# Optimization experiments

Measured on AMD Instinct MI355X. Metric: run time of the kernel, lower is better.

Reference implementation:

```python
import jax, jax.numpy as jnp
import numpy as np

N_NODES = 50000
N_EDGES = 800000
F_IN = 128          # num_features
F_HID = 128 * 3     # conv1 out
F_OUT = 256         # num_relations = num_criteria**2
N_CRIT = 16         # num_criteria


def setup_inputs() -> dict:
    key = jax.random.key(0)
    k_feat, k_edge, k_w1, k_w2 = jax.random.split(key, 4)
    features = jax.random.normal(k_feat, (N_NODES, F_IN), dtype=jnp.float32)
    edge_index = jax.random.randint(k_edge, (2, N_EDGES), 0, N_NODES, dtype=jnp.int32)
    # Glorot-ish init like dglnn.GraphConv
    W1 = jax.random.normal(k_w1, (F_IN, F_HID), dtype=jnp.float32) * (1.0 / np.sqrt(F_IN))
    b1 = jnp.zeros((F_HID,), dtype=jnp.float32)
    W2 = jax.random.normal(k_w2, (F_HID, F_OUT), dtype=jnp.float32) * (1.0 / np.sqrt(F_HID))
    b2 = jnp.zeros((F_OUT,), dtype=jnp.float32)
    return {"features": features, "W1": W1, "b1": b1, "W2": W2, "b2": b2,
            "edge_index": edge_index}


def reference(features, W1, b1, W2, b2, edge_index):
    src, dst = edge_index[0], edge_index[1]
    ones = jnp.ones((edge_index.shape[1],), dtype=features.dtype)
    # symmetric GCN norm with degrees clamped to min 1 (DGL norm='both')
    deg_out = jax.ops.segment_sum(ones, src, num_segments=N_NODES)
    deg_in = jax.ops.segment_sum(ones, dst, num_segments=N_NODES)
    out_norm = jnp.clip(deg_out, 1.0, None) ** -0.5   # [N]
    in_norm = jnp.clip(deg_in, 1.0, None) ** -0.5     # [N]

    def aggregate(h):
        # h: [N, d] -> D_in^{-1/2} A D_out^{-1/2} h  via edge gather + segment_sum
        msg = (h * out_norm[:, None])[src]                              # [E, d]
        return jax.ops.segment_sum(msg, dst, num_segments=N_NODES) * in_norm[:, None]

    # conv1: in(128) < out(384) -> aggregate first, then dense transform
    x = jax.nn.relu(aggregate(features) @ W1 + b1)      # [N, 384]
    # conv2: in(384) > out(256) -> dense transform first, then aggregate
    x = aggregate(x @ W2) + b2                          # [N, 256]
    return x.reshape(-1, N_CRIT, N_CRIT)                # [N, 16, 16]
```

## Files before the change

kernel.cpp:

```cpp
#include <hip/hip_runtime.h>
#include <hip/hip_bf16.h>

typedef float f32x4 __attribute__((ext_vector_type(4)));
typedef __bf16 bf16x8 __attribute__((ext_vector_type(8)));

#define NNODES 50000
#define NEDGES 800000
#define FIN 128
#define FHID 384
#define FOUT 256

#define SCAN_NB ((NNODES + 1023) / 1024)

__device__ __forceinline__ float bf_lo(unsigned u) { return __uint_as_float(u << 16); }
__device__ __forceinline__ float bf_hi(unsigned u) { return __uint_as_float(u & 0xffff0000u); }
__device__ __forceinline__ unsigned short f2bf(float f) {
  unsigned u = __float_as_uint(f);
  u += 0x7fffu + ((u >> 16) & 1u);
  return (unsigned short)(u >> 16);
}

__global__ void cvt_feat_kernel(const float* __restrict__ f,
                                const float* __restrict__ onorm,
                                unsigned short* __restrict__ o, int n4) {
  int i = blockIdx.x * blockDim.x + threadIdx.x;
  if (i >= n4) return;
  float4 v = *(const float4*)(f + (size_t)i * 4);
  float w = onorm[(i * 4) >> 7];
  ushort4 r;
  r.x = f2bf(v.x * w); r.y = f2bf(v.y * w);
  r.z = f2bf(v.z * w); r.w = f2bf(v.w * w);
  *(ushort4*)(o + (size_t)i * 4) = r;
}

__global__ void wt_kernel(const float* __restrict__ W, __bf16* __restrict__ Wt, int K, int Nw) {
  int i = blockIdx.x * blockDim.x + threadIdx.x;
  if (i >= K * Nw) return;
  int k = i / Nw, n = i % Nw;
  unsigned short b = f2bf(W[i]);
  Wt[(size_t)n * K + k] = *(__bf16*)&b;
}

__global__ void degree_kernel(const int* __restrict__ ei, int* __restrict__ dout, int* __restrict__ din) {
  int e = blockIdx.x * blockDim.x + threadIdx.x;
  if (e >= NEDGES) return;
  atomicAdd(&dout[ei[e]], 1);
  atomicAdd(&din[ei[NEDGES + e]], 1);
}

__global__ void norm_kernel(const int* __restrict__ dout, const int* __restrict__ din,
                            float* __restrict__ onorm, float* __restrict__ inorm) {
  int i = blockIdx.x * blockDim.x + threadIdx.x;
  if (i >= NNODES) return;
  int a = dout[i]; if (a < 1) a = 1;
  int b = din[i]; if (b < 1) b = 1;
  onorm[i] = rsqrtf((float)a);
  inorm[i] = rsqrtf((float)b);
}

__global__ __launch_bounds__(256) void scan_part1(const int* __restrict__ deg,
                                                  int* __restrict__ blocksums) {
  int b = blockIdx.x, t = threadIdx.x;
  int base = b * 1024 + t * 4;
  int s = 0;
  if (base + 4 <= NNODES) {
    int4 v = *(const int4*)(deg + base);
    s = v.x + v.y + v.z + v.w;
  } else {
    for (int j = 0; j < 4; ++j)
      if (base + j < NNODES) s += deg[base + j];
  }
  for (int d = 32; d >= 1; d >>= 1) s += __shfl_down(s, d, 64);
  __shared__ int ws[4];
  int lane = t & 63, w = t >> 6;
  if (lane == 0) ws[w] = s;
  __syncthreads();
  if (t == 0) blocksums[b] = ws[0] + ws[1] + ws[2] + ws[3];
}

__global__ void scan_mid(const int* __restrict__ bs, int* __restrict__ boff) {
  int t = threadIdx.x;
  int v = (t < SCAN_NB) ? bs[t] : 0;
  int x = v;
  for (int d = 1; d < 64; d <<= 1) {
    int y = __shfl_up(x, d, 64);
    if (t >= d) x += y;
  }
  if (t < SCAN_NB) boff[t] = x - v;
}

__global__ __launch_bounds__(256) void scan_part2(const int* __restrict__ deg,
                                                  const int* __restrict__ boff,
                                                  int* __restrict__ row_ptr,
                                                  int* __restrict__ cursor) {
  int b = blockIdx.x, t = threadIdx.x;
  int base = b * 1024 + t * 4;
  int v0 = 0, v1 = 0, v2 = 0, v3 = 0;
  if (base + 4 <= NNODES) {
    int4 v = *(const int4*)(deg + base);
    v0 = v.x; v1 = v.y; v2 = v.z; v3 = v.w;
  } else {
    if (base + 0 < NNODES) v0 = deg[base + 0];
    if (base + 1 < NNODES) v1 = deg[base + 1];
    if (base + 2 < NNODES) v2 = deg[base + 2];
    if (base + 3 < NNODES) v3 = deg[base + 3];
  }
  int s = v0 + v1 + v2 + v3;
  int x = s;
  int lane = t & 63, w = t >> 6;
  for (int d = 1; d < 64; d <<= 1) {
    int y = __shfl_up(x, d, 64);
    if (lane >= d) x += y;
  }
  __shared__ int ws[4];
  if (lane == 63) ws[w] = x;
  __syncthreads();
  int woff = 0;
  for (int i = 0; i < w; ++i) woff += ws[i];
  int off = boff[b] + woff + (x - s);
  if (base + 0 < NNODES) { row_ptr[base + 0] = off; cursor[base + 0] = off; off += v0; }
  if (base + 1 < NNODES) { row_ptr[base + 1] = off; cursor[base + 1] = off; off += v1; }
  if (base + 2 < NNODES) { row_ptr[base + 2] = off; cursor[base + 2] = off; off += v2; }
  if (base + 3 < NNODES) { row_ptr[base + 3] = off; cursor[base + 3] = off; off += v3; }
  if (base < NNODES && base + 4 >= NNODES) row_ptr[NNODES] = off;
}

__global__ void fill_kernel(const int* __restrict__ ei, int* __restrict__ cursor, int* __restrict__ csr) {
  int e = blockIdx.x * blockDim.x + threadIdx.x;
  if (e >= NEDGES) return;
  int d = ei[NEDGES + e];
  int pos = atomicAdd(&cursor[d], 1);
  csr[pos] = ei[e];
}

__global__ __launch_bounds__(256) void agg1_kernel(
    const int* __restrict__ row_ptr, const int* __restrict__ csr,
    const float* __restrict__ inorm, const unsigned short* __restrict__ featb,
    unsigned short* __restrict__ aggF) {
  int node = (blockIdx.x << 2) + (threadIdx.x >> 6);
  if (node >= NNODES) return;
  int lane = threadIdx.x & 63;
  int quarter = lane >> 4;
  int fl8 = (lane & 15) << 3;
  const unsigned short* tab = featb + fl8;
  int beg = row_ptr[node], end = row_ptr[node + 1];
  float a0 = 0.f, a1 = 0.f, a2 = 0.f, a3 = 0.f, a4 = 0.f, a5 = 0.f, a6 = 0.f, a7 = 0.f;
  int e = beg;
  for (; e + 8 <= end; e += 8) {
    int s0 = csr[e + quarter];
    int s1 = csr[e + 4 + quarter];
    uint4 v0 = *(const uint4*)(tab + (size_t)s0 * FIN);
    uint4 v1 = *(const uint4*)(tab + (size_t)s1 * FIN);
    a0 += bf_lo(v0.x); a1 += bf_hi(v0.x); a2 += bf_lo(v0.y); a3 += bf_hi(v0.y);
    a4 += bf_lo(v0.z); a5 += bf_hi(v0.z); a6 += bf_lo(v0.w); a7 += bf_hi(v0.w);
    a0 += bf_lo(v1.x); a1 += bf_hi(v1.x); a2 += bf_lo(v1.y); a3 += bf_hi(v1.y);
    a4 += bf_lo(v1.z); a5 += bf_hi(v1.z); a6 += bf_lo(v1.w); a7 += bf_hi(v1.w);
  }
  for (int t = e + quarter; t < end; t += 4) {
    int s0 = csr[t];
    uint4 v0 = *(const uint4*)(tab + (size_t)s0 * FIN);
    a0 += bf_lo(v0.x); a1 += bf_hi(v0.x); a2 += bf_lo(v0.y); a3 += bf_hi(v0.y);
    a4 += bf_lo(v0.z); a5 += bf_hi(v0.z); a6 += bf_lo(v0.w); a7 += bf_hi(v0.w);
  }
  a0 += __shfl_xor(a0, 16, 64); a1 += __shfl_xor(a1, 16, 64);
  a2 += __shfl_xor(a2, 16, 64); a3 += __shfl_xor(a3, 16, 64);
  a4 += __shfl_xor(a4, 16, 64); a5 += __shfl_xor(a5, 16, 64);
  a6 += __shfl_xor(a6, 16, 64); a7 += __shfl_xor(a7, 16, 64);
  a0 += __shfl_xor(a0, 32, 64); a1 += __shfl_xor(a1, 32, 64);
  a2 += __shfl_xor(a2, 32, 64); a3 += __shfl_xor(a3, 32, 64);
  a4 += __shfl_xor(a4, 32, 64); a5 += __shfl_xor(a5, 32, 64);
  a6 += __shfl_xor(a6, 32, 64); a7 += __shfl_xor(a7, 32, 64);
  float p0 = (quarter == 0) ? a0 : (quarter == 1) ? a2 : (quarter == 2) ? a4 : a6;
  float p1 = (quarter == 0) ? a1 : (quarter == 1) ? a3 : (quarter == 2) ? a5 : a7;
  float inn = inorm[node];
  unsigned pk = (unsigned)f2bf(p0 * inn) | ((unsigned)f2bf(p1 * inn) << 16);
  *(unsigned*)(aggF + (size_t)node * FIN + fl8 + (quarter << 1)) = pk;
}

__global__ __launch_bounds__(256) void agg2_kernel(
    const int* __restrict__ row_ptr, const int* __restrict__ csr,
    const float* __restrict__ inorm, const unsigned short* __restrict__ h2s,
    const float* __restrict__ b2, float* __restrict__ out) {
  int node = (blockIdx.x << 2) + (threadIdx.x >> 6);
  if (node >= NNODES) return;
  int lane = threadIdx.x & 63;
  int half = lane >> 5;
  int fl8 = (lane & 31) << 3;
  const unsigned short* tab = h2s + fl8;
  int beg = row_ptr[node], end = row_ptr[node + 1];
  float a0 = 0.f, a1 = 0.f, a2 = 0.f, a3 = 0.f, a4 = 0.f, a5 = 0.f, a6 = 0.f, a7 = 0.f;
  int e = beg;
  for (; e + 4 <= end; e += 4) {
    int s0 = csr[e + half];
    int s1 = csr[e + 2 + half];
    uint4 v0 = *(const uint4*)(tab + (size_t)s0 * FOUT);
    uint4 v1 = *(const uint4*)(tab + (size_t)s1 * FOUT);
    a0 += bf_lo(v0.x); a1 += bf_hi(v0.x); a2 += bf_lo(v0.y); a3 += bf_hi(v0.y);
    a4 += bf_lo(v0.z); a5 += bf_hi(v0.z); a6 += bf_lo(v0.w); a7 += bf_hi(v0.w);
    a0 += bf_lo(v1.x); a1 += bf_hi(v1.x); a2 += bf_lo(v1.y); a3 += bf_hi(v1.y);
    a4 += bf_lo(v1.z); a5 += bf_hi(v1.z); a6 += bf_lo(v1.w); a7 += bf_hi(v1.w);
  }
  for (int t = e + half; t < end; t += 2) {
    int s0 = csr[t];
    uint4 v0 = *(const uint4*)(tab + (size_t)s0 * FOUT);
    a0 += bf_lo(v0.x); a1 += bf_hi(v0.x); a2 += bf_lo(v0.y); a3 += bf_hi(v0.y);
    a4 += bf_lo(v0.z); a5 += bf_hi(v0.z); a6 += bf_lo(v0.w); a7 += bf_hi(v0.w);
  }
  a0 += __shfl_xor(a0, 32, 64); a1 += __shfl_xor(a1, 32, 64);
  a2 += __shfl_xor(a2, 32, 64); a3 += __shfl_xor(a3, 32, 64);
  a4 += __shfl_xor(a4, 32, 64); a5 += __shfl_xor(a5, 32, 64);
  a6 += __shfl_xor(a6, 32, 64); a7 += __shfl_xor(a7, 32, 64);
  float q0 = half ? a4 : a0;
  float q1 = half ? a5 : a1;
  float q2 = half ? a6 : a2;
  float q3 = half ? a7 : a3;
  int f = fl8 + (half << 2);
  float inn = inorm[node];
  float4 bv = *(const float4*)(b2 + f);
  float4 r;
  r.x = fmaf(q0, inn, bv.x);
  r.y = fmaf(q1, inn, bv.y);
  r.z = fmaf(q2, inn, bv.z);
  r.w = fmaf(q3, inn, bv.w);
  *(float4*)(out + (size_t)node * FOUT + f) = r;
}

__device__ __forceinline__ f32x4 mfma16(bf16x8 a, bf16x8 b, f32x4 c) {
  return __builtin_amdgcn_mfma_f32_16x16x32_bf16(a, b, c, 0, 0, 0);
}

__global__ __launch_bounds__(256) void gemm_bf16(
    const __bf16* __restrict__ A, const __bf16* __restrict__ Bt,
    const float* __restrict__ bias, const float* __restrict__ row_scale,
    __bf16* __restrict__ C, int M, int N, int K, int relu) {
  __shared__ __attribute__((aligned(16))) __bf16 As[128 * 64];
  __shared__ __attribute__((aligned(16))) __bf16 Bs[128 * 64];
  const int tid = threadIdx.x;
  const int lane = tid & 63;
  const int wave = tid >> 6;
  const int wm = (wave >> 1) << 6;
  const int wn = (wave & 1) << 6;
  const int r16 = lane & 15;
  const int kg = lane >> 4;
  const int m0 = blockIdx.x * 128;
  const int n0 = blockIdx.y * 128;
  f32x4 acc[4][4];
#pragma unroll
  for (int m = 0; m < 4; ++m)
#pragma unroll
    for (int n = 0; n < 4; ++n) acc[m][n] = f32x4{0.f, 0.f, 0.f, 0.f};

  for (int k0 = 0; k0 < K; k0 += 64) {
    __syncthreads();
#pragma unroll
    for (int i = 0; i < 4; ++i) {
      int c = tid + (i << 8);
      int row = c >> 3;
      int col = c & 7;
      int sw = ((col ^ (row & 7)) << 3);
      int ga = m0 + row;
      uint4 av = make_uint4(0u, 0u, 0u, 0u);
      if (ga < M) av = *(const uint4*)(A + (size_t)ga * K + k0 + (col << 3));
      *(uint4*)(As + row * 64 + sw) = av;
      uint4 bv = *(const uint4*)(Bt + (size_t)(n0 + row) * K + k0 + (col << 3));
      *(uint4*)(Bs + row * 64 + sw) = bv;
    }
    __syncthreads();
#pragma unroll
    for (int kk = 0; kk < 2; ++kk) {
      int kc = (kk << 2) + kg;
      bf16x8 a[4], b[4];
#pragma unroll
      for (int m = 0; m < 4; ++m) {
        int r = wm + (m << 4) + r16;
        a[m] = *(const bf16x8*)(As + r * 64 + ((kc ^ (r & 7)) << 3));
      }
#pragma unroll
      for (int n = 0; n < 4; ++n) {
        int r = wn + (n << 4) + r16;
        b[n] = *(const bf16x8*)(Bs + r * 64 + ((kc ^ (r & 7)) << 3));
      }
#pragma unroll
      for (int m = 0; m < 4; ++m)
#pragma unroll
        for (int n = 0; n < 4; ++n)
          acc[m][n] = mfma16(a[m], b[n], acc[m][n]);
    }
  }
#pragma unroll
  for (int m = 0; m < 4; ++m) {
#pragma unroll
    for (int j = 0; j < 4; ++j) {
      int row = m0 + wm + (m << 4) + (kg << 2) + j;
      if (row < M) {
        float sc = row_scale ? row_scale[row] : 1.f;
#pragma unroll
        for (int n = 0; n < 4; ++n) {
          int col = n0 + wn + (n << 4) + r16;
          float v = acc[m][n][j] + (bias ? bias[col] : 0.f);
          if (relu) v = fmaxf(v, 0.f);
          v *= sc;
          unsigned short h = f2bf(v);
          C[(size_t)row * N + col] = *(__bf16*)&h;
        }
      }
    }
  }
}

extern "C" void kernel_launch(void* const* d_in, const int* in_sizes, int n_in,
                              void* d_out, int out_size, void* d_ws, size_t ws_size,
                              hipStream_t stream) {
  const float* features = (const float*)d_in[0];
  const float* W1 = (const float*)d_in[1];
  const float* b1 = (const float*)d_in[2];
  const float* W2 = (const float*)d_in[3];
  const float* b2 = (const float*)d_in[4];
  const int* ei = (const int*)d_in[5];
  float* out = (float*)d_out;

  char* ws = (char*)d_ws;
  size_t off = 0;
  auto alloc = [&](size_t bytes) -> void* {
    void* p = ws + off;
    off += (bytes + 255) & ~(size_t)255;
    return p;
  };
  int* degi_out = (int*)alloc((size_t)NNODES * 4);
  int* degi_in  = (int*)alloc((size_t)NNODES * 4);
  float* onorm  = (float*)alloc((size_t)NNODES * 4);
  float* inorm  = (float*)alloc((size_t)NNODES * 4);
  int* row_ptr  = (int*)alloc((size_t)(NNODES + 1) * 4);
  int* cursor   = (int*)alloc((size_t)NNODES * 4);
  int* csr_src  = (int*)alloc((size_t)NEDGES * 4);
  int* blocksums = (int*)alloc((size_t)SCAN_NB * 4);
  int* blockoffs = (int*)alloc((size_t)SCAN_NB * 4);
  unsigned short* featb = (unsigned short*)alloc((size_t)NNODES * FIN * 2);
  unsigned short* aggF  = (unsigned short*)alloc((size_t)NNODES * FIN * 2);
  __bf16* h1  = (__bf16*)alloc((size_t)NNODES * FHID * 2);
  __bf16* h2s = (__bf16*)alloc((size_t)NNODES * FOUT * 2);
  __bf16* W1t = (__bf16*)alloc((size_t)FIN * FHID * 2);
  __bf16* W2t = (__bf16*)alloc((size_t)FHID * FOUT * 2);
  (void)ws_size; (void)n_in; (void)in_sizes; (void)out_size;

  hipMemsetAsync(degi_out, 0, 2 * (((size_t)NNODES * 4 + 255) & ~(size_t)255), stream);

  degree_kernel<<<(NEDGES + 255) / 256, 256, 0, stream>>>(ei, degi_out, degi_in);
  norm_kernel<<<(NNODES + 255) / 256, 256, 0, stream>>>(degi_out, degi_in, onorm, inorm);
  scan_part1<<<SCAN_NB, 256, 0, stream>>>(degi_in, blocksums);
  scan_mid<<<1, 64, 0, stream>>>(blocksums, blockoffs);
  scan_part2<<<SCAN_NB, 256, 0, stream>>>(degi_in, blockoffs, row_ptr, cursor);
  fill_kernel<<<(NEDGES + 255) / 256, 256, 0, stream>>>(ei, cursor, csr_src);

  cvt_feat_kernel<<<(NNODES * FIN / 4 + 255) / 256, 256, 0, stream>>>(
      features, onorm, featb, NNODES * FIN / 4);
  wt_kernel<<<(FIN * FHID + 255) / 256, 256, 0, stream>>>(W1, W1t, FIN, FHID);
  wt_kernel<<<(FHID * FOUT + 255) / 256, 256, 0, stream>>>(W2, W2t, FHID, FOUT);

  agg1_kernel<<<(NNODES + 3) / 4, 256, 0, stream>>>(
      row_ptr, csr_src, inorm, featb, aggF);
  gemm_bf16<<<dim3((NNODES + 127) / 128, FHID / 128), 256, 0, stream>>>(
      (const __bf16*)aggF, W1t, b1, nullptr, h1, NNODES, FHID, FIN, 1);

  gemm_bf16<<<dim3((NNODES + 127) / 128, FOUT / 128), 256, 0, stream>>>(
      h1, W2t, nullptr, onorm, h2s, NNODES, FOUT, FHID, 0);
  agg2_kernel<<<(NNODES + 3) / 4, 256, 0, stream>>>(
      row_ptr, csr_src, inorm, (const unsigned short*)h2s, b2, out);
}
```

Measured before the change: 377.7 us.

## Build CSR via per-block LDS histograms and ranks instead of global atomics

```diff
diff --git a/kernel.cpp b/kernel.cpp
--- a/kernel.cpp
+++ b/kernel.cpp
@@ -11,6 +11,10 @@
 #define FOUT 256
 
 #define SCAN_NB ((NNODES + 1023) / 1024)
+
+#define HB 64
+#define EPB (NEDGES / HB)
+#define HW (NNODES / 2)
 
 __device__ __forceinline__ float bf_lo(unsigned u) { return __uint_as_float(u << 16); }
 __device__ __forceinline__ float bf_hi(unsigned u) { return __uint_as_float(u & 0xffff0000u); }
@@ -41,21 +45,57 @@
   Wt[(size_t)n * K + k] = *(__bf16*)&b;
 }
 
-__global__ void degree_kernel(const int* __restrict__ ei, int* __restrict__ dout, int* __restrict__ din) {
-  int e = blockIdx.x * blockDim.x + threadIdx.x;
-  if (e >= NEDGES) return;
-  atomicAdd(&dout[ei[e]], 1);
-  atomicAdd(&din[ei[NEDGES + e]], 1);
-}
-
-__global__ void norm_kernel(const int* __restrict__ dout, const int* __restrict__ din,
-                            float* __restrict__ onorm, float* __restrict__ inorm) {
-  int i = blockIdx.x * blockDim.x + threadIdx.x;
-  if (i >= NNODES) return;
-  int a = dout[i]; if (a < 1) a = 1;
-  int b = din[i]; if (b < 1) b = 1;
-  onorm[i] = rsqrtf((float)a);
-  inorm[i] = rsqrtf((float)b);
+__global__ __launch_bounds__(256) void hist_kernel(
+    const int* __restrict__ ei, unsigned* __restrict__ psrc,
+    unsigned* __restrict__ pdst, unsigned short* __restrict__ rank) {
+  __shared__ unsigned hist[HW];
+  int b = blockIdx.x, pass = blockIdx.y, t = threadIdx.x;
+  for (int i = t; i < HW; i += 256) hist[i] = 0;
+  __syncthreads();
+  const int* idx = ei + (pass ? NEDGES : 0) + b * EPB;
+  if (pass == 0) {
+    for (int i = t; i < EPB; i += 256) {
+      int n = idx[i];
+      atomicAdd(&hist[n >> 1], 1u << ((n & 1) << 4));
+    }
+  } else {
+    for (int i = t; i < EPB; i += 256) {
+      int n = idx[i];
+      unsigned sh = (n & 1) << 4;
+      unsigned old = atomicAdd(&hist[n >> 1], 1u << sh);
+      rank[b * EPB + i] = (unsigned short)((old >> sh) & 0xFFFFu);
+    }
+  }
+  __syncthreads();
+  unsigned* dst = (pass ? pdst : psrc) + (size_t)b * HW;
+  for (int i = t; i < HW; i += 256) dst[i] = hist[i];
+}
+
+__global__ __launch_bounds__(256) void reduce_hist(
+    const unsigned* __restrict__ psrc, unsigned* __restrict__ pdst,
+    int* __restrict__ din, float* __restrict__ onorm, float* __restrict__ inorm) {
+  int w = blockIdx.x * blockDim.x + threadIdx.x;
+  if (w >= HW) return;
+  unsigned sl = 0, sh = 0;
+#pragma unroll 8
+  for (int b = 0; b < HB; ++b) {
+    unsigned v = psrc[(size_t)b * HW + w];
+    sl += v & 0xFFFFu; sh += v >> 16;
+  }
+  unsigned rl = 0, rh = 0;
+#pragma unroll 8
+  for (int b = 0; b < HB; ++b) {
+    size_t o = (size_t)b * HW + w;
+    unsigned v = pdst[o];
+    pdst[o] = rl | (rh << 16);
+    rl += v & 0xFFFFu; rh += v >> 16;
+  }
+  int n0 = 2 * w, n1 = 2 * w + 1;
+  din[n0] = (int)rl; din[n1] = (int)rh;
+  onorm[n0] = rsqrtf((float)(sl ? sl : 1u));
+  onorm[n1] = rsqrtf((float)(sh ? sh : 1u));
+  inorm[n0] = rsqrtf((float)(rl ? rl : 1u));
+  inorm[n1] = rsqrtf((float)(rh ? rh : 1u));
 }
 
 __global__ __launch_bounds__(256) void scan_part1(const int* __restrict__ deg,
@@ -91,8 +131,7 @@
 
 __global__ __launch_bounds__(256) void scan_part2(const int* __restrict__ deg,
                                                   const int* __restrict__ boff,
-                                                  int* __restrict__ row_ptr,
-                                                  int* __restrict__ cursor) {
+                                                  int* __restrict__ row_ptr) {
   int b = blockIdx.x, t = threadIdx.x;
   int base = b * 1024 + t * 4;
   int v0 = 0, v1 = 0, v2 = 0, v3 = 0;
@@ -118,19 +157,24 @@
   int woff = 0;
   for (int i = 0; i < w; ++i) woff += ws[i];
   int off = boff[b] + woff + (x - s);
-  if (base + 0 < NNODES) { row_ptr[base + 0] = off; cursor[base + 0] = off; off += v0; }
-  if (base + 1 < NNODES) { row_ptr[base + 1] = off; cursor[base + 1] = off; off += v1; }
-  if (base + 2 < NNODES) { row_ptr[base + 2] = off; cursor[base + 2] = off; off += v2; }
-  if (base + 3 < NNODES) { row_ptr[base + 3] = off; cursor[base + 3] = off; off += v3; }
+  if (base + 0 < NNODES) { row_ptr[base + 0] = off; off += v0; }
+  if (base + 1 < NNODES) { row_ptr[base + 1] = off; off += v1; }
+  if (base + 2 < NNODES) { row_ptr[base + 2] = off; off += v2; }
+  if (base + 3 < NNODES) { row_ptr[base + 3] = off; off += v3; }
   if (base < NNODES && base + 4 >= NNODES) row_ptr[NNODES] = off;
 }
 
-__global__ void fill_kernel(const int* __restrict__ ei, int* __restrict__ cursor, int* __restrict__ csr) {
+__global__ void fill_kernel(const int* __restrict__ ei,
+                            const unsigned short* __restrict__ rank,
+                            const unsigned* __restrict__ pdst,
+                            const int* __restrict__ row_ptr,
+                            int* __restrict__ csr) {
   int e = blockIdx.x * blockDim.x + threadIdx.x;
   if (e >= NEDGES) return;
-  int d = ei[NEDGES + e];
-  int pos = atomicAdd(&cursor[d], 1);
-  csr[pos] = ei[e];
+  int n = ei[NEDGES + e];
+  int b = e / EPB;
+  unsigned base = (pdst[(size_t)b * HW + (n >> 1)] >> ((n & 1) << 4)) & 0xFFFFu;
+  csr[row_ptr[n] + (int)base + (int)rank[e]] = ei[e];
 }
 
 __global__ __launch_bounds__(256) void agg1_kernel(
@@ -326,12 +370,10 @@
     off += (bytes + 255) & ~(size_t)255;
     return p;
   };
-  int* degi_out = (int*)alloc((size_t)NNODES * 4);
-  int* degi_in  = (int*)alloc((size_t)NNODES * 4);
   float* onorm  = (float*)alloc((size_t)NNODES * 4);
   float* inorm  = (float*)alloc((size_t)NNODES * 4);
+  int* din      = (int*)alloc((size_t)NNODES * 4);
   int* row_ptr  = (int*)alloc((size_t)(NNODES + 1) * 4);
-  int* cursor   = (int*)alloc((size_t)NNODES * 4);
   int* csr_src  = (int*)alloc((size_t)NEDGES * 4);
   int* blocksums = (int*)alloc((size_t)SCAN_NB * 4);
   int* blockoffs = (int*)alloc((size_t)SCAN_NB * 4);
@@ -343,14 +385,16 @@
   __bf16* W2t = (__bf16*)alloc((size_t)FHID * FOUT * 2);
   (void)ws_size; (void)n_in; (void)in_sizes; (void)out_size;
 
-  hipMemsetAsync(degi_out, 0, 2 * (((size_t)NNODES * 4 + 255) & ~(size_t)255), stream);
-
-  degree_kernel<<<(NEDGES + 255) / 256, 256, 0, stream>>>(ei, degi_out, degi_in);
-  norm_kernel<<<(NNODES + 255) / 256, 256, 0, stream>>>(degi_out, degi_in, onorm, inorm);
-  scan_part1<<<SCAN_NB, 256, 0, stream>>>(degi_in, blocksums);
+  unsigned* psrc = (unsigned*)h1;
+  unsigned* pdst = psrc + (size_t)HB * HW;
+  unsigned short* rank = (unsigned short*)(pdst + (size_t)HB * HW);
+
+  hist_kernel<<<dim3(HB, 2), 256, 0, stream>>>(ei, psrc, pdst, rank);
+  reduce_hist<<<(HW + 255) / 256, 256, 0, stream>>>(psrc, pdst, din, onorm, inorm);
+  scan_part1<<<SCAN_NB, 256, 0, stream>>>(din, blocksums);
   scan_mid<<<1, 64, 0, stream>>>(blocksums, blockoffs);
-  scan_part2<<<SCAN_NB, 256, 0, stream>>>(degi_in, blockoffs, row_ptr, cursor);
-  fill_kernel<<<(NEDGES + 255) / 256, 256, 0, stream>>>(ei, cursor, csr_src);
+  scan_part2<<<SCAN_NB, 256, 0, stream>>>(din, blockoffs, row_ptr);
+  fill_kernel<<<(NEDGES + 255) / 256, 256, 0, stream>>>(ei, rank, pdst, row_ptr, csr_src);
 
   cvt_feat_kernel<<<(NNODES * FIN / 4 + 255) / 256, 256, 0, stream>>>(
       features, onorm, featb, NNODES * FIN / 4);
```

Measured after the change: 313.2 us. 17.1% less time.
